# Kernel tuning notes

Measured on AMD Instinct MI355X. Metric: run time of the kernel, lower is better.

Reference implementation:

```python
import jax, jax.numpy as jnp
import numpy as np

P = 10                      # half-window; kernel size K = 2P+1 = 21
GROUPS = ((0, 1000), (1000, 2000))  # hardcoded self.group = [0, 1000, 2000]


def setup_inputs() -> dict:
    key = jax.random.key(0)
    k1, k2, k3 = jax.random.split(key, 3)
    n, T, D = 16, 1024, 2000
    x = jax.random.normal(k1, (n, T, D), dtype=jnp.float32)
    W0 = jax.random.normal(k2, (D, 2 * P + 1), dtype=jnp.float32)
    W1 = jax.random.normal(k3, (D, 2 * P + 1), dtype=jnp.float32)
    return {"x": x, "W0": W0, "W1": W1}


def _shift_attention(x, Ws):
    n, T, D = x.shape
    K = 2 * P + 1
    # x_padded built from the ORIGINAL x under no_grad (detached)
    xp = jax.lax.stop_gradient(jnp.pad(x, ((0, 0), (P, P), (0, 0))))
    cur = x
    for Wi, (s, e) in zip(Ws, GROUPS):
        # dynamic per-timestep window weights: (n, T, K)
        w = jnp.einsum('ntd,dk->ntk', cur, Wi)
        xg = xp[:, :, s:e]  # (n, T+2P, g)
        # out[:, t, :] = sum_k w[:, t, k] * xg[:, t+k, :]  (windowed combine)
        out = w[:, :, 0, None] * xg[:, 0:T, :]
        for k in range(1, K):  # fixed small tap count, not a data-dim loop
            out = out + w[:, :, k, None] * xg[:, k:k + T, :]
        # in-place column update -> group 1 sees group 0's result in 'cur'
        cur = cur.at[:, :, s:e].set(out)
    return cur


def reference(x, W0, W1):
    return _shift_attention(x, (W0, W1))
```

## Files before the change

kernel.cpp:

```cpp
#include <hip/hip_runtime.h>

#define N_  16
#define T_  1024
#define D_  2000
#define K_  21
#define P_  10
#define NT_ (N_*T_)

__global__ void k_padW(const float* __restrict__ W0, const float* __restrict__ W1,
                       float* __restrict__ W0p, float* __restrict__ W1p) {
    int gid = blockIdx.x * blockDim.x + threadIdx.x;
    if (gid >= D_ * 24) return;
    int d = gid / 24, kk = gid - d * 24;
    float v0 = (kk < K_) ? W0[d * K_ + kk] : 0.f;
    float v1 = (kk < K_) ? W1[d * K_ + kk] : 0.f;
    W0p[gid] = v0;
    W1p[gid] = v1;
}

__global__ __launch_bounds__(256)
void k_coef(const float* __restrict__ x,
            const float* __restrict__ W0p, const float* __restrict__ W1p,
            float* __restrict__ q0, float* __restrict__ q1,
            float* __restrict__ q2, float* __restrict__ q3,
            float* __restrict__ Ma, float* __restrict__ Mb,
            float* __restrict__ Pa, float* __restrict__ Pb) {
    __shared__ float red[256 * 22];
    const int tid  = threadIdx.x;
    const int lane = tid & 63;
    const int w    = tid >> 6;
    const int rg   = blockIdx.x >> 2;
    const int h    = blockIdx.x & 3;
    const int r    = rg * 64 + lane;

    const int starts[4] = {0, 128, 256, 384};
    const int widths[4] = {128, 128, 128, 116};
    const int ds = h * 500 + starts[w];
    const int n4 = widths[w] >> 2;

    float a0[K_], ab[K_];
#pragma unroll
    for (int k = 0; k < K_; ++k) { a0[k] = 0.f; ab[k] = 0.f; }

    const float* __restrict__ xr = x + (size_t)r * D_ + ds;

#pragma unroll 2
    for (int i = 0; i < n4; ++i) {
        const float4 xv = *reinterpret_cast<const float4*>(xr + i * 4);
        const int dbase = ds + i * 4;
#pragma unroll
        for (int j = 0; j < 4; ++j) {
            const int du = __builtin_amdgcn_readfirstlane(dbase + j);
            const float* __restrict__ wr0 = W0p + du * 24;
            const float* __restrict__ wr1 = W1p + du * 24;
            const float xs = (j == 0) ? xv.x : (j == 1) ? xv.y : (j == 2) ? xv.z : xv.w;
#pragma unroll
            for (int k = 0; k < K_; ++k) a0[k] = fmaf(xs, wr0[k], a0[k]);
#pragma unroll
            for (int k = 0; k < K_; ++k) ab[k] = fmaf(xs, wr1[k], ab[k]);
        }
    }

    float* const w0dst[4] = {q0, q1, q2, q3};
    float* const mpdst[4] = {Ma, Mb, Pa, Pb};

#pragma unroll
    for (int k = 0; k < K_; ++k) red[tid * 22 + k] = a0[k];
    __syncthreads();
    for (int o = tid; o < 64 * K_; o += 256) {
        int t = o / K_, j = o - t * K_;
        float s = red[t * 22 + j] + red[(64 + t) * 22 + j] +
                  red[(128 + t) * 22 + j] + red[(192 + t) * 22 + j];
        w0dst[h][(size_t)(rg * 64 + t) * K_ + j] = s;
    }
    __syncthreads();
#pragma unroll
    for (int k = 0; k < K_; ++k) red[tid * 22 + k] = ab[k];
    __syncthreads();
    for (int o = tid; o < 64 * K_; o += 256) {
        int t = o / K_, j = o - t * K_;
        float s = red[t * 22 + j] + red[(64 + t) * 22 + j] +
                  red[(128 + t) * 22 + j] + red[(192 + t) * 22 + j];
        mpdst[h][(size_t)(rg * 64 + t) * K_ + j] = s;
    }
}

__global__ void k_finish(const float* __restrict__ q0, const float* __restrict__ q1,
                         const float* __restrict__ q2, const float* __restrict__ q3,
                         const float* __restrict__ Ma, const float* __restrict__ Mb,
                         const float* __restrict__ Pa, const float* __restrict__ Pb,
                         float* __restrict__ w0f, float* __restrict__ w1f) {
    int o = blockIdx.x * blockDim.x + threadIdx.x;
    if (o >= NT_ * K_) return;
    int row = o / K_, k = o - row * K_;
    int t = row & (T_ - 1);

    const size_t rb = (size_t)row * K_;
    float w0row[K_];
#pragma unroll
    for (int j = 0; j < K_; ++j)
        w0row[j] = q0[rb + j] + q1[rb + j] + q2[rb + j] + q3[rb + j];
    w0f[o] = w0row[k];

    float acc = Pa[o] + Pb[o];
#pragma unroll
    for (int j = 0; j < K_; ++j) {
        int tt = t + j - P_;
        if (tt >= 0 && tt < T_) {
            size_t ro = (size_t)(row + j - P_) * K_ + k;
            acc = fmaf(w0row[j], Ma[ro] + Mb[ro], acc);
        }
    }
    w1f[o] = acc;
}

__global__ __launch_bounds__(256)
void k_conv(const float* __restrict__ x, const float* __restrict__ w0,
            const float* __restrict__ w1, float* __restrict__ out) {
    __shared__ float xsl[84][128];
    __shared__ float wc[64 * K_];
    const int b = blockIdx.x;
    const int grp = b >> 11;
    const float* __restrict__ coef = grp ? w1 : w0;
    const int dbase = grp * 1000;
    const int bb = b & 2047;
    const int dseg = bb & 7;
    const int tch = (bb >> 3) & 15;
    const int nn = bb >> 7;
    const int t0 = tch * 64;
    const int tid = threadIdx.x;
    const float* xb = x + (size_t)nn * T_ * D_;

    {
        const int scol = tid & 31, srow0 = tid >> 5;
#pragma unroll
        for (int pass = 0; pass < 11; ++pass) {
            int rr = srow0 + pass * 8;
            if (rr < 84) {
                int u = t0 - P_ + rr;
                int dl = dseg * 128 + scol * 4;
                float4 v = make_float4(0.f, 0.f, 0.f, 0.f);
                if (u >= 0 && u < T_ && dl < 1000)
                    v = *reinterpret_cast<const float4*>(xb + (size_t)u * D_ + dbase + dl);
                *reinterpret_cast<float4*>(&xsl[rr][scol * 4]) = v;
            }
        }
    }
    for (int o = tid; o < 64 * K_; o += 256) {
        int tl = o / K_, k = o - tl * K_;
        wc[o] = coef[((size_t)nn * T_ + t0 + tl) * K_ + k];
    }
    __syncthreads();

    const int col = tid & 31;
    const int tsub = tid >> 5;
    const int tl0 = tsub * 8;
    float4 acc[8];
#pragma unroll
    for (int g = 0; g < 8; ++g) acc[g] = make_float4(0.f, 0.f, 0.f, 0.f);

#pragma unroll
    for (int ul = 0; ul < 28; ++ul) {
        const int rr = tl0 + ul;
        const float4 xf = *reinterpret_cast<const float4*>(&xsl[rr][col * 4]);
#pragma unroll
        for (int g = 0; g < 8; ++g) {
            const int k = ul - g;
            if (k >= 0 && k < K_) {
                const float c = wc[(tl0 + g) * K_ + k];
                acc[g].x = fmaf(c, xf.x, acc[g].x);
                acc[g].y = fmaf(c, xf.y, acc[g].y);
                acc[g].z = fmaf(c, xf.z, acc[g].z);
                acc[g].w = fmaf(c, xf.w, acc[g].w);
            }
        }
    }

    const int dl = dseg * 128 + col * 4;
    if (dl < 1000) {
#pragma unroll
        for (int g = 0; g < 8; ++g) {
            float* dst = out + ((size_t)nn * T_ + t0 + tl0 + g) * D_ + dbase + dl;
            *reinterpret_cast<float4*>(dst) = acc[g];
        }
    }
}

extern "C" void kernel_launch(void* const* d_in, const int* in_sizes, int n_in,
                              void* d_out, int out_size, void* d_ws, size_t ws_size,
                              hipStream_t stream) {
    const float* x  = (const float*)d_in[0];
    const float* W0 = (const float*)d_in[1];
    const float* W1 = (const float*)d_in[2];
    float* out = (float*)d_out;
    float* ws  = (float*)d_ws;

    const size_t CW = 344064;
    float* W0p = ws;
    float* W1p = ws + 48000;
    float* q0  = ws + 96000 + 0 * CW;
    float* q1  = ws + 96000 + 1 * CW;
    float* q2  = ws + 96000 + 2 * CW;
    float* q3  = ws + 96000 + 3 * CW;
    float* Ma  = ws + 96000 + 4 * CW;
    float* Mb  = ws + 96000 + 5 * CW;
    float* Pa  = ws + 96000 + 6 * CW;
    float* Pb  = ws + 96000 + 7 * CW;
    float* w0f = ws + 96000 + 8 * CW;
    float* w1f = ws + 96000 + 9 * CW;

    hipLaunchKernelGGL(k_padW, dim3(188), dim3(256), 0, stream, W0, W1, W0p, W1p);
    hipLaunchKernelGGL(k_coef, dim3(1024), dim3(256), 0, stream,
                       x, W0p, W1p, q0, q1, q2, q3, Ma, Mb, Pa, Pb);
    hipLaunchKernelGGL(k_finish, dim3(1344), dim3(256), 0, stream,
                       q0, q1, q2, q3, Ma, Mb, Pa, Pb, w0f, w1f);
    hipLaunchKernelGGL(k_conv, dim3(4096), dim3(256), 0, stream, x, w0f, w1f, out);
}
```

Before: 388.4 us.

## Stage x tiles through LDS with double buffering in coefficient kernel and tile finish kernel

```diff
diff --git a/kernel.cpp b/kernel.cpp
--- a/kernel.cpp
+++ b/kernel.cpp
@@ -12,10 +12,8 @@
     int gid = blockIdx.x * blockDim.x + threadIdx.x;
     if (gid >= D_ * 24) return;
     int d = gid / 24, kk = gid - d * 24;
-    float v0 = (kk < K_) ? W0[d * K_ + kk] : 0.f;
-    float v1 = (kk < K_) ? W1[d * K_ + kk] : 0.f;
-    W0p[gid] = v0;
-    W1p[gid] = v1;
+    W0p[gid] = (kk < K_) ? W0[d * K_ + kk] : 0.f;
+    W1p[gid] = (kk < K_) ? W1[d * K_ + kk] : 0.f;
 }
 
 __global__ __launch_bounds__(256)
@@ -23,95 +21,132 @@
             const float* __restrict__ W0p, const float* __restrict__ W1p,
             float* __restrict__ q0, float* __restrict__ q1,
             float* __restrict__ q2, float* __restrict__ q3,
-            float* __restrict__ Ma, float* __restrict__ Mb,
-            float* __restrict__ Pa, float* __restrict__ Pb) {
-    __shared__ float red[256 * 22];
+            float* __restrict__ m0, float* __restrict__ m1,
+            float* __restrict__ p1, float* __restrict__ p2,
+            float* __restrict__ p3) {
+    __shared__ float lds[5888];
     const int tid  = threadIdx.x;
     const int lane = tid & 63;
-    const int w    = tid >> 6;
+    const int w    = __builtin_amdgcn_readfirstlane(tid >> 6);
     const int rg   = blockIdx.x >> 2;
     const int h    = blockIdx.x & 3;
-    const int r    = rg * 64 + lane;
-
-    const int starts[4] = {0, 128, 256, 384};
-    const int widths[4] = {128, 128, 128, 116};
-    const int ds = h * 500 + starts[w];
-    const int n4 = widths[w] >> 2;
-
-    float a0[K_], ab[K_];
-#pragma unroll
-    for (int k = 0; k < K_; ++k) { a0[k] = 0.f; ab[k] = 0.f; }
-
-    const float* __restrict__ xr = x + (size_t)r * D_ + ds;
-
-#pragma unroll 2
-    for (int i = 0; i < n4; ++i) {
-        const float4 xv = *reinterpret_cast<const float4*>(xr + i * 4);
-        const int dbase = ds + i * 4;
-#pragma unroll
-        for (int j = 0; j < 4; ++j) {
-            const int du = __builtin_amdgcn_readfirstlane(dbase + j);
+    const int r0   = rg * 64;
+    const int d0q  = h * 512;
+
+    float a0[K_], am[K_], ap[K_];
+#pragma unroll
+    for (int k = 0; k < K_; ++k) { a0[k] = 0.f; am[k] = 0.f; ap[k] = 0.f; }
+
+    const int srow = tid >> 2;
+    const int sc4  = (tid & 3) * 2;
+    float4 ra, rb;
+
+    auto load_tile = [&](int dt) {
+        const int d = d0q + dt + sc4 * 4;
+        const float* p = x + (size_t)(r0 + srow) * D_ + d;
+        ra = (d     < D_) ? *reinterpret_cast<const float4*>(p)
+                          : make_float4(0.f, 0.f, 0.f, 0.f);
+        rb = (d + 4 < D_) ? *reinterpret_cast<const float4*>(p + 4)
+                          : make_float4(0.f, 0.f, 0.f, 0.f);
+    };
+    auto write_tile = [&](int buf) {
+        float* b = lds + buf * 2112 + srow * 33 + sc4 * 4;
+        b[0] = ra.x; b[1] = ra.y; b[2] = ra.z; b[3] = ra.w;
+        b[4] = rb.x; b[5] = rb.y; b[6] = rb.z; b[7] = rb.w;
+    };
+
+    load_tile(0);
+    write_tile(0);
+    __syncthreads();
+
+    for (int t = 0; t < 16; ++t) {
+        if (t < 15) load_tile((t + 1) * 32);
+        const float* xrow = lds + (t & 1) * 2112 + lane * 33;
+#pragma unroll
+        for (int c = 0; c < 8; ++c) {
+            const int col = w * 8 + c;
+            const int d = d0q + t * 32 + col;
+            const int du = (d < D_) ? d : (D_ - 1);
+            const float xv = xrow[col];
             const float* __restrict__ wr0 = W0p + du * 24;
             const float* __restrict__ wr1 = W1p + du * 24;
-            const float xs = (j == 0) ? xv.x : (j == 1) ? xv.y : (j == 2) ? xv.z : xv.w;
-#pragma unroll
-            for (int k = 0; k < K_; ++k) a0[k] = fmaf(xs, wr0[k], a0[k]);
-#pragma unroll
-            for (int k = 0; k < K_; ++k) ab[k] = fmaf(xs, wr1[k], ab[k]);
-        }
-    }
-
-    float* const w0dst[4] = {q0, q1, q2, q3};
-    float* const mpdst[4] = {Ma, Mb, Pa, Pb};
-
-#pragma unroll
-    for (int k = 0; k < K_; ++k) red[tid * 22 + k] = a0[k];
+#pragma unroll
+            for (int k = 0; k < K_; ++k) a0[k] = fmaf(xv, wr0[k], a0[k]);
+            if (d < 1000) {
+#pragma unroll
+                for (int k = 0; k < K_; ++k) am[k] = fmaf(xv, wr1[k], am[k]);
+            } else {
+#pragma unroll
+                for (int k = 0; k < K_; ++k) ap[k] = fmaf(xv, wr1[k], ap[k]);
+            }
+        }
+        if (t < 15) write_tile((t + 1) & 1);
+        __syncthreads();
+    }
+
+    auto reduce_store = [&](const float* acc, float* dst) {
+        __syncthreads();
+#pragma unroll
+        for (int k = 0; k < K_; ++k) lds[tid * 23 + k] = acc[k];
+        __syncthreads();
+        for (int o = tid; o < 64 * K_; o += 256) {
+            int t = o / K_, j = o - t * K_;
+            float s = lds[t * 23 + j] + lds[(64 + t) * 23 + j] +
+                      lds[(128 + t) * 23 + j] + lds[(192 + t) * 23 + j];
+            dst[(size_t)(r0 + t) * K_ + j] = s;
+        }
+    };
+
+    float* const qd[4] = {q0, q1, q2, q3};
+    reduce_store(a0, qd[h]);
+    if (h == 0) reduce_store(am, m0);
+    if (h == 1) { reduce_store(am, m1); reduce_store(ap, p1); }
+    if (h == 2) reduce_store(ap, p2);
+    if (h == 3) reduce_store(ap, p3);
+}
+
+__global__ __launch_bounds__(256)
+void k_finish(const float* __restrict__ q0, const float* __restrict__ q1,
+              const float* __restrict__ q2, const float* __restrict__ q3,
+              const float* __restrict__ m0, const float* __restrict__ m1,
+              const float* __restrict__ p1, const float* __restrict__ p2,
+              const float* __restrict__ p3,
+              float* __restrict__ w0f, float* __restrict__ w1f) {
+    __shared__ float w0s[64 * K_];
+    __shared__ float Ms[84 * K_];
+    const int tid = threadIdx.x;
+    const int r0 = blockIdx.x * 64;
+
+    for (int o = tid; o < 64 * K_; o += 256) {
+        size_t g = (size_t)r0 * K_ + o;
+        w0s[o] = q0[g] + q1[g] + q2[g] + q3[g];
+    }
+    for (int o = tid; o < 84 * K_; o += 256) {
+        int i = o / K_, j = o - i * K_;
+        int rr = r0 - P_ + i;
+        float v = 0.f;
+        if (rr >= 0 && rr < NT_) {
+            size_t g = (size_t)rr * K_ + j;
+            v = m0[g] + m1[g];
+        }
+        Ms[o] = v;
+    }
     __syncthreads();
+
     for (int o = tid; o < 64 * K_; o += 256) {
-        int t = o / K_, j = o - t * K_;
-        float s = red[t * 22 + j] + red[(64 + t) * 22 + j] +
-                  red[(128 + t) * 22 + j] + red[(192 + t) * 22 + j];
-        w0dst[h][(size_t)(rg * 64 + t) * K_ + j] = s;
-    }
-    __syncthreads();
-#pragma unroll
-    for (int k = 0; k < K_; ++k) red[tid * 22 + k] = ab[k];
-    __syncthreads();
-    for (int o = tid; o < 64 * K_; o += 256) {
-        int t = o / K_, j = o - t * K_;
-        float s = red[t * 22 + j] + red[(64 + t) * 22 + j] +
-                  red[(128 + t) * 22 + j] + red[(192 + t) * 22 + j];
-        mpdst[h][(size_t)(rg * 64 + t) * K_ + j] = s;
-    }
-}
-
-__global__ void k_finish(const float* __restrict__ q0, const float* __restrict__ q1,
-                         const float* __restrict__ q2, const float* __restrict__ q3,
-                         const float* __restrict__ Ma, const float* __restrict__ Mb,
-                         const float* __restrict__ Pa, const float* __restrict__ Pb,
-                         float* __restrict__ w0f, float* __restrict__ w1f) {
-    int o = blockIdx.x * blockDim.x + threadIdx.x;
-    if (o >= NT_ * K_) return;
-    int row = o / K_, k = o - row * K_;
-    int t = row & (T_ - 1);
-
-    const size_t rb = (size_t)row * K_;
-    float w0row[K_];
-#pragma unroll
-    for (int j = 0; j < K_; ++j)
-        w0row[j] = q0[rb + j] + q1[rb + j] + q2[rb + j] + q3[rb + j];
-    w0f[o] = w0row[k];
-
-    float acc = Pa[o] + Pb[o];
-#pragma unroll
-    for (int j = 0; j < K_; ++j) {
-        int tt = t + j - P_;
-        if (tt >= 0 && tt < T_) {
-            size_t ro = (size_t)(row + j - P_) * K_ + k;
-            acc = fmaf(w0row[j], Ma[ro] + Mb[ro], acc);
-        }
-    }
-    w1f[o] = acc;
+        int row = o / K_, k = o - row * K_;
+        size_t g = (size_t)(r0 + row) * K_ + k;
+        float acc = p1[g] + p2[g] + p3[g];
+        int t = (r0 + row) & (T_ - 1);
+#pragma unroll
+        for (int j = 0; j < K_; ++j) {
+            int tt = t + j - P_;
+            if (tt >= 0 && tt < T_)
+                acc = fmaf(w0s[row * K_ + j], Ms[(row + j) * K_ + k], acc);
+        }
+        w1f[g] = acc;
+        w0f[g] = w0s[o];
+    }
 }
 
 __global__ __launch_bounds__(256)
@@ -202,17 +237,18 @@
     float* q1  = ws + 96000 + 1 * CW;
     float* q2  = ws + 96000 + 2 * CW;
     float* q3  = ws + 96000 + 3 * CW;
-    float* Ma  = ws + 96000 + 4 * CW;
-    float* Mb  = ws + 96000 + 5 * CW;
-    float* Pa  = ws + 96000 + 6 * CW;
-    float* Pb  = ws + 96000 + 7 * CW;
-    float* w0f = ws + 96000 + 8 * CW;
-    float* w1f = ws + 96000 + 9 * CW;
+    float* m0  = ws + 96000 + 4 * CW;
+    float* m1  = ws + 96000 + 5 * CW;
+    float* p1  = ws + 96000 + 6 * CW;
+    float* p2  = ws + 96000 + 7 * CW;
+    float* p3  = ws + 96000 + 8 * CW;
+    float* w0f = ws + 96000 + 9 * CW;
+    float* w1f = ws + 96000 + 10 * CW;
 
     hipLaunchKernelGGL(k_padW, dim3(188), dim3(256), 0, stream, W0, W1, W0p, W1p);
     hipLaunchKernelGGL(k_coef, dim3(1024), dim3(256), 0, stream,
-                       x, W0p, W1p, q0, q1, q2, q3, Ma, Mb, Pa, Pb);
-    hipLaunchKernelGGL(k_finish, dim3(1344), dim3(256), 0, stream,
-                       q0, q1, q2, q3, Ma, Mb, Pa, Pb, w0f, w1f);
+                       x, W0p, W1p, q0, q1, q2, q3, m0, m1, p1, p2, p3);
+    hipLaunchKernelGGL(k_finish, dim3(256), dim3(256), 0, stream,
+                       q0, q1, q2, q3, m0, m1, p1, p2, p3, w0f, w1f);
     hipLaunchKernelGGL(k_conv, dim3(4096), dim3(256), 0, stream, x, w0f, w1f, out);
 }
```

Measured after the change: 468.6 us. 20.7% more time.
